# Performance work log

Hardware: AMD Instinct MI355X
Metric: run time of the kernel (lower is better)

Reference implementation:

```python
import jax, jax.numpy as jnp
import numpy as np

MARGIN = 0.1
SCALE_POS = 2.0
SCALE_NEG = 50.0
THRESH = 0.5
EPS = 1e-5


def setup_inputs() -> dict:
    key = jax.random.key(0)
    k1, k2 = jax.random.split(key)
    feats = jax.random.normal(k1, (4096, 2, 192), dtype=jnp.float32)
    labels = jax.random.randint(k2, (4096,), 0, 4096, dtype=jnp.int64)
    return {"feats": feats, "labels": labels}


def reference(feats, labels):
    B, n_utt, D = feats.shape
    lab = jnp.repeat(labels, n_utt)            # [N]
    f = feats.reshape(-1, D)                   # [N, D]
    N = f.shape[0]

    sim = f @ f.T                              # [N, N]
    # F.normalize(sim): L2-normalize each row, eps=1e-12
    row_norm = jnp.maximum(jnp.linalg.norm(sim, axis=1, keepdims=True), 1e-12)
    S = sim / row_norm

    same = lab[None, :] == lab[:, None]        # [N, N]
    pos_mask = same & (S < 1.0 - EPS)          # pos_pair_ (includes self if < 1-eps)
    neg_mask = ~same                           # neg_pair_

    min_pos = jnp.min(jnp.where(pos_mask, S, jnp.inf), axis=1)    # per-row min(pos_pair_)
    max_neg = jnp.max(jnp.where(neg_mask, S, -jnp.inf), axis=1)   # per-row max(neg_pair_)

    neg_keep = neg_mask & (S > (min_pos - MARGIN)[:, None])
    pos_keep = pos_mask & (S < (max_neg + MARGIN)[:, None])

    has_neg = jnp.any(neg_keep, axis=1)
    has_pos = jnp.any(pos_keep, axis=1)
    valid = has_neg & has_pos

    pos_sum = jnp.sum(jnp.where(pos_keep, jnp.exp(-SCALE_POS * (S - THRESH)), 0.0), axis=1)
    neg_sum = jnp.sum(jnp.where(neg_keep, jnp.exp(SCALE_NEG * (S - THRESH)), 0.0), axis=1)

    row_loss = (1.0 / SCALE_POS) * jnp.log1p(pos_sum) + (1.0 / SCALE_NEG) * jnp.log1p(neg_sum)
    loss = jnp.sum(jnp.where(valid, row_loss, 0.0)) / N

    # prec1 = percent of rows skipped for having no surviving negatives
    prec1 = jnp.sum(~has_neg).astype(jnp.float32) * 100.0 / N
    return loss, prec1
```

## Files before the change

kernel.cpp:

```cpp
#include <hip/hip_runtime.h>
#include <math.h>

typedef __bf16 bf16x8 __attribute__((ext_vector_type(8)));
typedef float  f32x4  __attribute__((ext_vector_type(4)));
typedef int    int4v  __attribute__((ext_vector_type(4)));

constexpr float MARGIN    = 0.1f;
constexpr float SCALE_POS = 2.0f;
constexpr float SCALE_NEG = 50.0f;
constexpr float THRESH    = 0.5f;
constexpr float ONE_EPS   = 1.0f - 1e-5f;
constexpr float LOG2E     = 1.4426950408889634f;
constexpr float BC        = -(SCALE_NEG * THRESH * LOG2E);
constexpr float VCUT_COEF = (36.0674f - 30.0f) / (SCALE_NEG * LOG2E);

constexpr int D      = 192;
constexpr int KS     = 6;
constexpr int RT     = 4;
constexpr int RPW    = 64;
constexpr int RPB    = 256;
constexpr int CSPLIT = 16;

constexpr int TILE_SH = KS * 64 * 8;

__device__ inline short f2bf(float x) {
  unsigned u = __float_as_uint(x);
  u += 0x7fffu + ((u >> 16) & 1u);
  return (short)(u >> 16);
}

__device__ inline float fast_exp2(float x) {
#if __has_builtin(__builtin_amdgcn_exp2f)
  return __builtin_amdgcn_exp2f(x);
#else
  return exp2f(x);
#endif
}

__global__ void k_pack(const float* __restrict__ f, short* __restrict__ pk, int total8) {
  int tid = blockIdx.x * blockDim.x + threadIdx.x;
  if (tid >= total8) return;
  int row = tid / 24;
  int j   = tid - row * 24;
  const float* src = f + (size_t)tid * 8;
  float4 a = *(const float4*)(src);
  float4 b = *(const float4*)(src + 4);
  union { short s[8]; int4v v; } o;
  o.s[0] = f2bf(a.x); o.s[1] = f2bf(a.y); o.s[2] = f2bf(a.z); o.s[3] = f2bf(a.w);
  o.s[4] = f2bf(b.x); o.s[5] = f2bf(b.y); o.s[6] = f2bf(b.z); o.s[7] = f2bf(b.w);
  int idx = (((row >> 4) * KS + (j >> 2)) * 64 + (j & 3) * 16 + (row & 15)) * 8;
  *(int4v*)(pk + idx) = o.v;
}

__global__ __launch_bounds__(1024) void k_buckets(
    const int* __restrict__ labs, int* __restrict__ hist_g, int* __restrict__ offs_g,
    int* __restrict__ bucket, float* __restrict__ accum, int n)
{
  __shared__ int histL[4096];
  __shared__ int offsL[4096];
  __shared__ int scanb[1024];
  const int t = threadIdx.x;

  if (t < 2) accum[t] = 0.f;
  for (int i = t; i < 4096; i += 1024) histL[i] = 0;
  __syncthreads();
  for (int i = t; i < n; i += 1024) atomicAdd(&histL[labs[i]], 1);
  __syncthreads();
  int base = t * 4;
  int v[4]; int ls = 0;
  for (int k = 0; k < 4; ++k) { v[k] = ls; ls += histL[base + k]; }
  scanb[t] = ls;
  __syncthreads();
  for (int o = 1; o < 1024; o <<= 1) {
    int x = (t >= o) ? scanb[t - o] : 0;
    __syncthreads();
    scanb[t] += x;
    __syncthreads();
  }
  int ebase = scanb[t] - ls;
  for (int k = 0; k < 4; ++k) {
    offsL[base + k] = ebase + v[k];
    offs_g[base + k] = ebase + v[k];
    hist_g[base + k] = histL[base + k];
  }
  __syncthreads();
  for (int i = t; i < 4096; i += 1024) histL[i] = 0;
  __syncthreads();
  for (int i = t; i < n; i += 1024) {
    int lab = labs[i];
    int p = atomicAdd(&histL[lab], 1);
    bucket[offsL[lab] + p] = i;
  }
}

__global__ __launch_bounds__(256, 2) void k_pass1(
    const short* __restrict__ pk, const int* __restrict__ labs,
    float* __restrict__ sumsqP, float* __restrict__ maxnegP,
    int N, int cps)
{
  const int lane = threadIdx.x & 63;
  const int w    = threadIdx.x >> 6;
  const int q    = lane >> 4;
  const int c    = lane & 15;
  const int cs   = blockIdx.x & (CSPLIT - 1);
  const int rbb  = blockIdx.x / CSPLIT;
  const int rowbase = rbb * RPB + w * RPW;
  const int col0 = cs * cps;

  bf16x8 afr[RT][KS];
#pragma unroll
  for (int rt = 0; rt < RT; ++rt)
#pragma unroll
    for (int ks = 0; ks < KS; ++ks)
      afr[rt][ks] = *(const bf16x8*)(pk + (size_t)((rowbase >> 4) + rt) * TILE_SH + (ks * 64 + lane) * 8);

  int labrow[RT][4];
#pragma unroll
  for (int rt = 0; rt < RT; ++rt)
#pragma unroll
    for (int rr = 0; rr < 4; ++rr)
      labrow[rt][rr] = labs[(rowbase + rt * 16 + q * 4 + rr) >> 1];

  float ssq[RT][4], mxn[RT][4];
#pragma unroll
  for (int rt = 0; rt < RT; ++rt)
#pragma unroll
    for (int rr = 0; rr < 4; ++rr) { ssq[rt][rr] = 0.f; mxn[rt][rr] = -INFINITY; }

  const short* bp = pk + (size_t)(col0 >> 4) * TILE_SH + lane * 8;
  for (int ct = 0; ct < cps; ct += 16, bp += TILE_SH) {
    const int labcol = labs[(col0 + ct + c) >> 1];
    bf16x8 bfr[KS];
#pragma unroll
    for (int ks = 0; ks < KS; ++ks) bfr[ks] = *(const bf16x8*)(bp + ks * 512);
    f32x4 acc[RT];
#pragma unroll
    for (int rt = 0; rt < RT; ++rt) acc[rt] = 0.f;
#pragma unroll
    for (int ks = 0; ks < KS; ++ks)
#pragma unroll
      for (int rt = 0; rt < RT; ++rt)
        acc[rt] = __builtin_amdgcn_mfma_f32_16x16x32_bf16(afr[rt][ks], bfr[ks], acc[rt], 0, 0, 0);
#pragma unroll
    for (int rt = 0; rt < RT; ++rt)
#pragma unroll
      for (int rr = 0; rr < 4; ++rr) {
        float v = acc[rt][rr];
        ssq[rt][rr] = fmaf(v, v, ssq[rt][rr]);
        float vm = (labrow[rt][rr] == labcol) ? -INFINITY : v;
        mxn[rt][rr] = fmaxf(mxn[rt][rr], vm);
      }
  }

#pragma unroll
  for (int rt = 0; rt < RT; ++rt)
#pragma unroll
    for (int rr = 0; rr < 4; ++rr) {
      float s = ssq[rt][rr], m = mxn[rt][rr];
#pragma unroll
      for (int msk = 1; msk < 16; msk <<= 1) {
        s += __shfl_xor(s, msk, 64);
        m = fmaxf(m, __shfl_xor(m, msk, 64));
      }
      if (c == 0) {
        int row = rowbase + rt * 16 + q * 4 + rr;
        sumsqP[(size_t)cs * N + row] = s;
        maxnegP[(size_t)cs * N + row] = m;
      }
    }
}

__global__ void k_rowstats(
    const float* __restrict__ f, const int* __restrict__ labs,
    const float* __restrict__ sumsqP, const float* __restrict__ maxnegP,
    const int* __restrict__ offs, const int* __restrict__ hist, const int* __restrict__ bucket,
    float* __restrict__ nthr2, float* __restrict__ arow,
    float* __restrict__ validf, float* __restrict__ hasnegf, float* __restrict__ posloss,
    int N)
{
  const int lane = threadIdx.x & 63;
  const int row  = blockIdx.x * 4 + (threadIdx.x >> 6);

  float s = 0.f, m = -INFINITY;
  if (lane < CSPLIT) {
    s = sumsqP[(size_t)lane * N + row];
    m = maxnegP[(size_t)lane * N + row];
  }
#pragma unroll
  for (int msk = 1; msk < 64; msk <<= 1) {
    s += __shfl_xor(s, msk, 64);
    m = fmaxf(m, __shfl_xor(m, msk, 64));
  }
  float nrm = fmaxf(sqrtf(s), 1e-12f);
  float inv = 1.0f / nrm;
  float maxnegS = m * inv;
  float posth = fminf(ONE_EPS, maxnegS + MARGIN);

  const int lab = labs[row >> 1];
  const int beg = offs[lab], cnt = hist[lab];
  const float* fi = f + (size_t)row * D;
  float x0 = fi[lane], x1 = fi[lane + 64], x2 = fi[lane + 128];

  float minp = INFINITY, psum = 0.f; int pcnt = 0;
  for (int t = 0; t < cnt; ++t) {
    int smp = bucket[beg + t];
#pragma unroll
    for (int u = 0; u < 2; ++u) {
      const float* fj = f + (size_t)(smp * 2 + u) * D;
      float p = x0 * fj[lane] + x1 * fj[lane + 64] + x2 * fj[lane + 128];
#pragma unroll
      for (int msk = 1; msk < 64; msk <<= 1) p += __shfl_xor(p, msk, 64);
      minp = fminf(minp, p);
      float S = p * inv;
      if (S < posth) {
        psum += fast_exp2((THRESH - S) * (SCALE_POS * LOG2E));
        pcnt++;
      }
    }
  }

  float minS = minp * inv;
  float min_pos = (minS < ONE_EPS) ? minS : INFINITY;
  bool hneg = maxnegS > (min_pos - MARGIN);
  bool valid = hneg && (pcnt > 0);
  if (lane == 0) {
    nthr2[row]   = fmaxf((min_pos - MARGIN) * nrm, VCUT_COEF * nrm);
    arow[row]    = inv * (SCALE_NEG * LOG2E);
    validf[row]  = valid ? 1.f : 0.f;
    hasnegf[row] = hneg ? 1.f : 0.f;
    posloss[row] = valid ? ((1.0f / SCALE_POS) * log1pf(psum)) : 0.f;
  }
}

__global__ __launch_bounds__(256, 2) void k_pass2(
    const short* __restrict__ pk,
    const float* __restrict__ nthr2, const float* __restrict__ arow,
    const float* __restrict__ maxnegP,
    float* __restrict__ negsumP, int N, int cps)
{
  const int lane = threadIdx.x & 63;
  const int w    = threadIdx.x >> 6;
  const int q    = lane >> 4;
  const int c    = lane & 15;
  const int cs   = blockIdx.x & (CSPLIT - 1);
  const int rbb  = blockIdx.x / CSPLIT;
  const int rowbase = rbb * RPB + w * RPW;
  const int col0 = cs * cps;

  {
    int myrow = rowbase + lane;
    float mn = maxnegP[(size_t)cs * N + myrow];
    float th = nthr2[myrow];
    unsigned long long bal = __ballot(mn > th);
    if (bal == 0ull) {
      negsumP[(size_t)cs * N + myrow] = 0.f;
      return;
    }
  }

  bf16x8 afr[RT][KS];
#pragma unroll
  for (int rt = 0; rt < RT; ++rt)
#pragma unroll
    for (int ks = 0; ks < KS; ++ks)
      afr[rt][ks] = *(const bf16x8*)(pk + (size_t)((rowbase >> 4) + rt) * TILE_SH + (ks * 64 + lane) * 8);

  float nthrv[RT][4], arw[RT][4], ns[RT][4];
#pragma unroll
  for (int rt = 0; rt < RT; ++rt)
#pragma unroll
    for (int rr = 0; rr < 4; ++rr) {
      int row = rowbase + rt * 16 + q * 4 + rr;
      nthrv[rt][rr] = nthr2[row];
      arw[rt][rr]   = arow[row];
      ns[rt][rr]    = 0.f;
    }

  const short* bp = pk + (size_t)(col0 >> 4) * TILE_SH + lane * 8;
  for (int ct = 0; ct < cps; ct += 16, bp += TILE_SH) {
    bf16x8 bfr[KS];
#pragma unroll
    for (int ks = 0; ks < KS; ++ks) bfr[ks] = *(const bf16x8*)(bp + ks * 512);
    f32x4 acc[RT];
#pragma unroll
    for (int rt = 0; rt < RT; ++rt) acc[rt] = 0.f;
#pragma unroll
    for (int ks = 0; ks < KS; ++ks)
#pragma unroll
      for (int rt = 0; rt < RT; ++rt)
        acc[rt] = __builtin_amdgcn_mfma_f32_16x16x32_bf16(afr[rt][ks], bfr[ks], acc[rt], 0, 0, 0);
#pragma unroll
    for (int rt = 0; rt < RT; ++rt)
#pragma unroll
      for (int rr = 0; rr < 4; ++rr) {
        float v = acc[rt][rr];
        float e = fast_exp2(fmaf(v, arw[rt][rr], BC));
        ns[rt][rr] += (v > nthrv[rt][rr]) ? e : 0.f;
      }
  }

#pragma unroll
  for (int rt = 0; rt < RT; ++rt)
#pragma unroll
    for (int rr = 0; rr < 4; ++rr) {
      float sv = ns[rt][rr];
#pragma unroll
      for (int msk = 1; msk < 16; msk <<= 1) sv += __shfl_xor(sv, msk, 64);
      if (c == 0) {
        int row = rowbase + rt * 16 + q * 4 + rr;
        negsumP[(size_t)cs * N + row] = sv;
      }
    }
}

__global__ void k_final_part(const float* __restrict__ negsumP, const float* __restrict__ posloss,
                             const float* __restrict__ validf, const float* __restrict__ hasnegf,
                             float* __restrict__ accum, int N)
{
  int i = blockIdx.x * blockDim.x + threadIdx.x;
  float lacc = 0.f, nacc = 0.f;
  if (i < N) {
    float nsum = 0.f;
    for (int cs2 = 0; cs2 < CSPLIT; ++cs2) nsum += negsumP[(size_t)cs2 * N + i];
    lacc = validf[i] * (posloss[i] + (1.0f / SCALE_NEG) * log1pf(nsum));
    nacc = 1.0f - hasnegf[i];
  }
#pragma unroll
  for (int msk = 1; msk < 64; msk <<= 1) {
    lacc += __shfl_xor(lacc, msk, 64);
    nacc += __shfl_xor(nacc, msk, 64);
  }
  __shared__ float sl[4], sn[4];
  int wid = threadIdx.x >> 6, lane = threadIdx.x & 63;
  if (lane == 0) { sl[wid] = lacc; sn[wid] = nacc; }
  __syncthreads();
  if (threadIdx.x == 0) {
    float L = sl[0] + sl[1] + sl[2] + sl[3];
    float Nn = sn[0] + sn[1] + sn[2] + sn[3];
    atomicAdd(&accum[0], L);
    atomicAdd(&accum[1], Nn);
  }
}

__global__ void k_write(const float* __restrict__ accum, float* __restrict__ out, int N) {
  out[0] = accum[0] / (float)N;
  out[1] = accum[1] * 100.0f / (float)N;
}

extern "C" void kernel_launch(void* const* d_in, const int* in_sizes, int n_in,
                              void* d_out, int out_size, void* d_ws, size_t ws_size,
                              hipStream_t stream)
{
  (void)n_in; (void)out_size; (void)ws_size;
  const float* f    = (const float*)d_in[0];
  const int*   labs = (const int*)d_in[1];
  const int Bs = in_sizes[1];
  const int N  = 2 * Bs;

  char* ws = (char*)d_ws;
  size_t off = 0;
  auto alloc = [&](size_t bytes) -> void* {
    void* p = ws + off;
    off += (bytes + 255) & ~(size_t)255;
    return p;
  };
  short* pk      = (short*)alloc((size_t)N * D * sizeof(short));
  float* sumsqP  = (float*)alloc((size_t)CSPLIT * N * sizeof(float));
  float* maxnegP = (float*)alloc((size_t)CSPLIT * N * sizeof(float));
  float* negsumP = (float*)alloc((size_t)CSPLIT * N * sizeof(float));
  float* nthr2   = (float*)alloc((size_t)N * sizeof(float));
  float* arow    = (float*)alloc((size_t)N * sizeof(float));
  float* validf  = (float*)alloc((size_t)N * sizeof(float));
  float* hasnegf = (float*)alloc((size_t)N * sizeof(float));
  float* posloss = (float*)alloc((size_t)N * sizeof(float));
  int* hist   = (int*)alloc((size_t)Bs * sizeof(int));
  int* offs   = (int*)alloc((size_t)Bs * sizeof(int));
  int* bucket = (int*)alloc((size_t)Bs * sizeof(int));
  float* accum = (float*)alloc(2 * sizeof(float));

  const int total8 = N * 24;
  k_pack<<<(total8 + 255) / 256, 256, 0, stream>>>(f, pk, total8);
  k_buckets<<<1, 1024, 0, stream>>>(labs, hist, offs, bucket, accum, Bs);

  const int cps   = N / CSPLIT;
  const int grid1 = (N / RPB) * CSPLIT;
  k_pass1<<<grid1, 256, 0, stream>>>(pk, labs, sumsqP, maxnegP, N, cps);
  k_rowstats<<<N / 4, 256, 0, stream>>>(f, labs, sumsqP, maxnegP, offs, hist, bucket,
                                        nthr2, arow, validf, hasnegf, posloss, N);
  k_pass2<<<grid1, 256, 0, stream>>>(pk, nthr2, arow, maxnegP, negsumP, N, cps);
  k_final_part<<<(N + 255) / 256, 256, 0, stream>>>(negsumP, posloss, validf, hasnegf, accum, N);
  k_write<<<1, 1, 0, stream>>>(accum, (float*)d_out, N);
}
```

Measured before the change: 119.0 us.

## Double-buffer B tiles in LDS via async global_load_lds in pass1

In pass1, each wave's column-tile B fragments are now prefetched with async global-to-LDS copies into a per-wave double buffer, so the next tile's load overlaps the current tile's MFMA work. Column labels are staged once into LDS instead of being read from global memory every iteration. The A fragments are pinned in registers with an empty asm to stop the compiler rematerializing them. The change adds LDS usage, which may limit occupancy, and relies on vmcnt waits rather than barriers because each wave owns its buffers. Each wave still loads its own copy of the B tile, so the loads are not shared across waves.

```diff
diff --git a/kernel.cpp b/kernel.cpp
--- a/kernel.cpp
+++ b/kernel.cpp
@@ -35,6 +35,18 @@
 #else
   return exp2f(x);
 #endif
+}
+
+__device__ inline void async_copy16(const short* g, short* l) {
+  __builtin_amdgcn_global_load_lds(
+      (const __attribute__((address_space(1))) unsigned int*)(const void*)g,
+      (__attribute__((address_space(3))) unsigned int*)(void*)l, 16, 0, 0);
+}
+
+__device__ inline void pin_frag(bf16x8& v) {
+  int4v t = __builtin_bit_cast(int4v, v);
+  asm volatile("" : "+v"(t));
+  v = __builtin_bit_cast(bf16x8, t);
 }
 
 __global__ void k_pack(const float* __restrict__ f, short* __restrict__ pk, int total8) {
@@ -98,21 +110,38 @@
     float* __restrict__ sumsqP, float* __restrict__ maxnegP,
     int N, int cps)
 {
-  const int lane = threadIdx.x & 63;
-  const int w    = threadIdx.x >> 6;
+  __shared__ short ldsB[4][2][KS * 512];
+  __shared__ int   ldsLab[512];
+
+  const int tid  = threadIdx.x;
+  const int lane = tid & 63;
+  const int w    = tid >> 6;
   const int q    = lane >> 4;
   const int c    = lane & 15;
   const int cs   = blockIdx.x & (CSPLIT - 1);
   const int rbb  = blockIdx.x / CSPLIT;
   const int rowbase = rbb * RPB + w * RPW;
   const int col0 = cs * cps;
+  const int ctile0 = col0 >> 4;
+  const int ntiles = cps >> 4;
+
+  for (int i = tid; i < cps; i += 256) ldsLab[i] = labs[(col0 + i) >> 1];
+
+  {
+    const short* g = pk + (size_t)ctile0 * TILE_SH + lane * 8;
+#pragma unroll
+    for (int k = 0; k < KS; ++k)
+      async_copy16(g + k * 512, &ldsB[w][0][k * 512]);
+  }
 
   bf16x8 afr[RT][KS];
 #pragma unroll
   for (int rt = 0; rt < RT; ++rt)
 #pragma unroll
-    for (int ks = 0; ks < KS; ++ks)
+    for (int ks = 0; ks < KS; ++ks) {
       afr[rt][ks] = *(const bf16x8*)(pk + (size_t)((rowbase >> 4) + rt) * TILE_SH + (ks * 64 + lane) * 8);
+      pin_frag(afr[rt][ks]);
+    }
 
   int labrow[RT][4];
 #pragma unroll
@@ -127,12 +156,21 @@
 #pragma unroll
     for (int rr = 0; rr < 4; ++rr) { ssq[rt][rr] = 0.f; mxn[rt][rr] = -INFINITY; }
 
-  const short* bp = pk + (size_t)(col0 >> 4) * TILE_SH + lane * 8;
-  for (int ct = 0; ct < cps; ct += 16, bp += TILE_SH) {
-    const int labcol = labs[(col0 + ct + c) >> 1];
+  __syncthreads();
+
+  for (int t = 0; t < ntiles; ++t) {
+    asm volatile("s_waitcnt vmcnt(0)" ::: "memory");
+    if (t + 1 < ntiles) {
+      const short* g = pk + (size_t)(ctile0 + t + 1) * TILE_SH + lane * 8;
+#pragma unroll
+      for (int k = 0; k < KS; ++k)
+        async_copy16(g + k * 512, &ldsB[w][(t + 1) & 1][k * 512]);
+    }
+    const int labcol = ldsLab[t * 16 + c];
     bf16x8 bfr[KS];
 #pragma unroll
-    for (int ks = 0; ks < KS; ++ks) bfr[ks] = *(const bf16x8*)(bp + ks * 512);
+    for (int ks = 0; ks < KS; ++ks)
+      bfr[ks] = *(const bf16x8*)&ldsB[w][t & 1][ks * 512 + lane * 8];
     f32x4 acc[RT];
 #pragma unroll
     for (int rt = 0; rt < RT; ++rt) acc[rt] = 0.f;
```

After: 121.0 us. No clear change (+1.6%).
